# Kernel tuning notes

Measured on AMD Instinct MI355X. Metric: run time of the kernel, lower is better.

## Reference

```python
import jax, jax.numpy as jnp
import numpy as np

VOCAB = 100000
DIM = 128
B = 32768
K = 16


def setup_inputs() -> dict:
    key = jax.random.key(0)
    k1, k2, k3, k4, k5 = jax.random.split(key, 5)
    init_range = 0.5 / DIM
    word_emb = jax.random.uniform(k1, (VOCAB, DIM), jnp.float32, -init_range, init_range)
    con_emb = jax.random.uniform(k2, (VOCAB, DIM), jnp.float32, -init_range, init_range)
    centrals_words = jax.random.randint(k3, (B,), 0, VOCAB, jnp.int64 if jax.config.jax_enable_x64 else jnp.int32)
    pos_context = jax.random.randint(k4, (B,), 0, VOCAB, centrals_words.dtype)
    neg_context = jax.random.randint(k5, (B, K), 0, VOCAB, centrals_words.dtype)
    return {
        "centrals_words": centrals_words,
        "pos_context": pos_context,
        "neg_context": neg_context,
        "word_emb": word_emb,
        "con_emb": con_emb,
    }


def reference(centrals_words, pos_context, neg_context, word_emb, con_emb):
    # Gathers
    w = word_emb[centrals_words]        # [B, D]
    c = con_emb[pos_context]            # [B, D]
    n = con_emb[neg_context]            # [B, K, D]
    # Positive score: dot over D
    pos_score = jnp.sum(w * c, axis=1)              # [B]
    pos_loss = jax.nn.log_sigmoid(pos_score)        # [B]
    # Negative scores: bmm [B,K,D] @ [B,D,1] -> [B,K]
    neg_score = jnp.einsum('bkd,bd->bk', n, w)      # [B, K]
    neg_loss = jnp.sum(jax.nn.log_sigmoid(-neg_score), axis=1)  # [B]
    loss = -jnp.mean(pos_loss + neg_loss)
    return loss
```

## Files before the change

### kernel.cpp

```cpp
#include <hip/hip_runtime.h>
#include <hip/hip_fp16.h>


constexpr int Bn = 32768;
constexpr int Kn = 16;
constexpr int WPB = 4;
constexpr int NBLK = Bn / WPB;
constexpr int VOCAB = 100000;
constexpr int DIM = 128;
constexpr size_t CONV_OFF = 65536;
constexpr float SCALE = 256.0f;
constexpr float INV_SCALE = 1.0f / 256.0f;

typedef float f32x2 __attribute__((ext_vector_type(2)));

__device__ __forceinline__ float log_sigmoid_fast(float x) {
  return fminf(x, 0.0f) - __logf(1.0f + __expf(-fabsf(x)));
}

template<int M, int C>
__device__ __forceinline__ void tree_step(float* v, int lane) {
  const bool hi = (lane & M) != 0;
  const int H = C / 2;
#pragma unroll
  for (int j = 0; j < H; ++j) {
    float send = hi ? v[j] : v[j + H];
    float keep = hi ? v[j + H] : v[j];
    v[j] = keep + __shfl_xor(send, M, 64);
  }
}

__device__ __forceinline__ f32x2 dec2_fp8(unsigned short t) {
  return __builtin_amdgcn_cvt_pk_f32_fp8((int)(unsigned int)t, false);
}

__global__ __launch_bounds__(256) void convert_con(
    const float4* __restrict__ in, unsigned int* __restrict__ out, int n4)
{
  int i = blockIdx.x * 256 + threadIdx.x;
  if (i >= n4) return;
  float4 v = in[i];
  int w = 0;
  w = __builtin_amdgcn_cvt_pk_fp8_f32(v.x * SCALE, v.y * SCALE, w, false);
  w = __builtin_amdgcn_cvt_pk_fp8_f32(v.z * SCALE, v.w * SCALE, w, true);
  out[i] = (unsigned int)w;
}

__global__ __launch_bounds__(256) void skipgram_main(
    const int* __restrict__ centrals,
    const int* __restrict__ pos_ctx,
    const int* __restrict__ neg_ctx,
    const float* __restrict__ word_emb,
    const unsigned short* __restrict__ con8,
    float* __restrict__ block_sums)
{
  const int lane = threadIdx.x & 63;
  int b = blockIdx.x * WPB + (threadIdx.x >> 6);
  b = __builtin_amdgcn_readfirstlane(b);

  const float2* __restrict__ W = reinterpret_cast<const float2*>(word_emb);

  const int cw = centrals[b];
  const int pc = pos_ctx[b];
  int ni[Kn];
#pragma unroll
  for (int k = 0; k < Kn; ++k) ni[k] = neg_ctx[b * Kn + k];

  const float2 wv = W[(size_t)cw * 64 + lane];
  const unsigned short cvb = con8[(size_t)pc * 64 + lane];
  unsigned short nvb[Kn];
#pragma unroll
  for (int k = 0; k < Kn; ++k) nvb[k] = con8[(size_t)ni[k] * 64 + lane];

  float v[Kn];
#pragma unroll
  for (int k = 0; k < Kn; ++k) {
    const f32x2 nf = dec2_fp8(nvb[k]);
    v[k] = fmaf(wv.x, nf.x, wv.y * nf.y);
  }

  tree_step<1, 16>(v, lane);
  tree_step<2,  8>(v, lane);
  tree_step<4,  4>(v, lane);
  tree_step<8,  2>(v, lane);
  float s = v[0];
  s += __shfl_xor(s, 16, 64);
  s += __shfl_xor(s, 32, 64);
  s *= INV_SCALE;

  float nls = log_sigmoid_fast(-s);
  nls += __shfl_xor(nls, 1, 64);
  nls += __shfl_xor(nls, 2, 64);
  nls += __shfl_xor(nls, 4, 64);
  nls += __shfl_xor(nls, 8, 64);

  const f32x2 cf = dec2_fp8(cvb);
  float pp = fmaf(wv.x, cf.x, wv.y * cf.y);
  pp += __shfl_xor(pp,  1, 64);
  pp += __shfl_xor(pp,  2, 64);
  pp += __shfl_xor(pp,  4, 64);
  pp += __shfl_xor(pp,  8, 64);
  pp += __shfl_xor(pp, 16, 64);
  pp += __shfl_xor(pp, 32, 64);
  pp *= INV_SCALE;

  const float acc = log_sigmoid_fast(pp) + nls;

  __shared__ float smem[WPB];
  if (lane == 0) smem[threadIdx.x >> 6] = acc;
  __syncthreads();
  if (threadIdx.x == 0)
    block_sums[blockIdx.x] = (smem[0] + smem[1]) + (smem[2] + smem[3]);
}

__global__ __launch_bounds__(256) void skipgram_reduce(
    const float* __restrict__ block_sums, float* __restrict__ out)
{
  float s = 0.0f;
#pragma unroll
  for (int i = 0; i < NBLK / 256; ++i) s += block_sums[i * 256 + threadIdx.x];
  s += __shfl_xor(s,  1, 64);
  s += __shfl_xor(s,  2, 64);
  s += __shfl_xor(s,  4, 64);
  s += __shfl_xor(s,  8, 64);
  s += __shfl_xor(s, 16, 64);
  s += __shfl_xor(s, 32, 64);
  __shared__ float smem[4];
  const int lane = threadIdx.x & 63;
  if (lane == 0) smem[threadIdx.x >> 6] = s;
  __syncthreads();
  if (threadIdx.x == 0) {
    float t = (smem[0] + smem[1]) + (smem[2] + smem[3]);
    out[0] = -t * (1.0f / (float)Bn);
  }
}

extern "C" void kernel_launch(void* const* d_in, const int* in_sizes, int n_in,
                              void* d_out, int out_size, void* d_ws, size_t ws_size,
                              hipStream_t stream) {
  const int*   centrals = (const int*)d_in[0];
  const int*   pos_ctx  = (const int*)d_in[1];
  const int*   neg_ctx  = (const int*)d_in[2];
  const float* word_emb = (const float*)d_in[3];
  const float* con_emb  = (const float*)d_in[4];
  float*       out      = (float*)d_out;

  float*        block_sums = (float*)d_ws;
  unsigned int* con_fp8 = (unsigned int*)((char*)d_ws + CONV_OFF);

  const int n4 = VOCAB * DIM / 4;
  convert_con<<<(n4 + 255) / 256, 256, 0, stream>>>(
      (const float4*)con_emb, con_fp8, n4);

  skipgram_main<<<NBLK, 256, 0, stream>>>(centrals, pos_ctx, neg_ctx,
                                          word_emb,
                                          (const unsigned short*)con_fp8,
                                          block_sums);

  skipgram_reduce<<<1, 256, 0, stream>>>(block_sums, out);
}
```

Measured before the change: 138.3 us.

## Remap lanes so each 16-lane group gathers four rows with wide vector loads

The wavefront is split into four 16-lane quarters. Each quarter handles four of the sixteen negative rows, and each lane loads 8 word floats as two float4s and 8 fp8 context bytes as one uint2. Before, every lane loaded a float2 and 17 separate 2-byte fp8 values. This cuts the number of small scattered load instructions and the shuffle-tree depth. In exchange, the positive dot product is computed redundantly in every quarter and the lane-to-row selection logic gets more complex.

```diff
diff --git a/kernel.cpp b/kernel.cpp
--- a/kernel.cpp
+++ b/kernel.cpp
@@ -30,8 +30,9 @@
   }
 }
 
-__device__ __forceinline__ f32x2 dec2_fp8(unsigned short t) {
-  return __builtin_amdgcn_cvt_pk_f32_fp8((int)(unsigned int)t, false);
+template<bool HI>
+__device__ __forceinline__ f32x2 dec2(unsigned int w) {
+  return __builtin_amdgcn_cvt_pk_f32_fp8((int)w, HI);
 }
 
 __global__ __launch_bounds__(256) void convert_con(
@@ -58,7 +59,8 @@
   int b = blockIdx.x * WPB + (threadIdx.x >> 6);
   b = __builtin_amdgcn_readfirstlane(b);
 
-  const float2* __restrict__ W = reinterpret_cast<const float2*>(word_emb);
+  const int m = lane & 15;
+  const int q = lane >> 4;
 
   const int cw = centrals[b];
   const int pc = pos_ctx[b];
@@ -66,42 +68,70 @@
 #pragma unroll
   for (int k = 0; k < Kn; ++k) ni[k] = neg_ctx[b * Kn + k];
 
-  const float2 wv = W[(size_t)cw * 64 + lane];
-  const unsigned short cvb = con8[(size_t)pc * 64 + lane];
-  unsigned short nvb[Kn];
+  const bool q1 = (q & 1) != 0;
+  const bool q2 = (q & 2) != 0;
+  int rowj[4];
 #pragma unroll
-  for (int k = 0; k < Kn; ++k) nvb[k] = con8[(size_t)ni[k] * 64 + lane];
-
-  float v[Kn];
-#pragma unroll
-  for (int k = 0; k < Kn; ++k) {
-    const f32x2 nf = dec2_fp8(nvb[k]);
-    v[k] = fmaf(wv.x, nf.x, wv.y * nf.y);
+  for (int j = 0; j < 4; ++j) {
+    int t0 = q1 ? ni[4 * j + 1] : ni[4 * j + 0];
+    int t1 = q1 ? ni[4 * j + 3] : ni[4 * j + 2];
+    rowj[j] = q2 ? t1 : t0;
   }
 
-  tree_step<1, 16>(v, lane);
-  tree_step<2,  8>(v, lane);
-  tree_step<4,  4>(v, lane);
-  tree_step<8,  2>(v, lane);
+  const float4* __restrict__ Wr =
+      reinterpret_cast<const float4*>(word_emb + (size_t)cw * DIM + m * 8);
+  const float4 wa = Wr[0];
+  const float4 wb = Wr[1];
+  const uint2 pv = *reinterpret_cast<const uint2*>(con8 + (size_t)pc * 64 + m * 4);
+  uint2 nv[4];
+#pragma unroll
+  for (int j = 0; j < 4; ++j)
+    nv[j] = *reinterpret_cast<const uint2*>(con8 + (size_t)rowj[j] * 64 + m * 4);
+
+  float v[4];
+#pragma unroll
+  for (int j = 0; j < 4; ++j) {
+    const f32x2 a0 = dec2<false>(nv[j].x);
+    const f32x2 a1 = dec2<true >(nv[j].x);
+    const f32x2 a2 = dec2<false>(nv[j].y);
+    const f32x2 a3 = dec2<true >(nv[j].y);
+    v[j] = fmaf(wa.x, a0.x,
+           fmaf(wa.y, a0.y,
+           fmaf(wa.z, a1.x,
+           fmaf(wa.w, a1.y,
+           fmaf(wb.x, a2.x,
+           fmaf(wb.y, a2.y,
+           fmaf(wb.z, a3.x, wb.w * a3.y)))))));
+  }
+
+  tree_step<1, 4>(v, lane);
+  tree_step<2, 2>(v, lane);
   float s = v[0];
-  s += __shfl_xor(s, 16, 64);
-  s += __shfl_xor(s, 32, 64);
+  s += __shfl_xor(s, 4, 64);
+  s += __shfl_xor(s, 8, 64);
   s *= INV_SCALE;
 
   float nls = log_sigmoid_fast(-s);
   nls += __shfl_xor(nls, 1, 64);
   nls += __shfl_xor(nls, 2, 64);
-  nls += __shfl_xor(nls, 4, 64);
-  nls += __shfl_xor(nls, 8, 64);
+  nls += __shfl_xor(nls, 16, 64);
+  nls += __shfl_xor(nls, 32, 64);
 
-  const f32x2 cf = dec2_fp8(cvb);
-  float pp = fmaf(wv.x, cf.x, wv.y * cf.y);
-  pp += __shfl_xor(pp,  1, 64);
-  pp += __shfl_xor(pp,  2, 64);
-  pp += __shfl_xor(pp,  4, 64);
-  pp += __shfl_xor(pp,  8, 64);
-  pp += __shfl_xor(pp, 16, 64);
-  pp += __shfl_xor(pp, 32, 64);
+  const f32x2 c0 = dec2<false>(pv.x);
+  const f32x2 c1 = dec2<true >(pv.x);
+  const f32x2 c2 = dec2<false>(pv.y);
+  const f32x2 c3 = dec2<true >(pv.y);
+  float pp = fmaf(wa.x, c0.x,
+             fmaf(wa.y, c0.y,
+             fmaf(wa.z, c1.x,
+             fmaf(wa.w, c1.y,
+             fmaf(wb.x, c2.x,
+             fmaf(wb.y, c2.y,
+             fmaf(wb.z, c3.x, wb.w * c3.y)))))));
+  pp += __shfl_xor(pp, 1, 64);
+  pp += __shfl_xor(pp, 2, 64);
+  pp += __shfl_xor(pp, 4, 64);
+  pp += __shfl_xor(pp, 8, 64);
   pp *= INV_SCALE;
 
   const float acc = log_sigmoid_fast(pp) + nls;
```

Result: slower. 163.7 us (+18.4%).

## Drop fp8 con_emb conversion pass and gather fp32 rows directly with persistent waves

Applied to the files above, without the earlier changes.

Removes the per-call kernel that converted the whole 100000x128 context table to scaled fp8, and instead gathers fp32 context rows directly. Only about 18 rows per sample are touched, so the full-table read and write is avoided at the cost of larger gathered rows. The main kernel now uses a fixed grid where each wave loops over several samples, with launch bounds raised to 8 blocks per CU. It also swaps some cross-lane shuffles for DPP moves and writes per-sample partial sums that a single-block kernel reduces.

```diff
diff --git a/kernel.cpp b/kernel.cpp
--- a/kernel.cpp
+++ b/kernel.cpp
@@ -1,21 +1,28 @@
 #include <hip/hip_runtime.h>
-#include <hip/hip_fp16.h>
 
 
 constexpr int Bn = 32768;
 constexpr int Kn = 16;
 constexpr int WPB = 4;
-constexpr int NBLK = Bn / WPB;
+constexpr int NBLK = 2048;
+constexpr int NWAVE = NBLK * WPB;
+constexpr int NITER = Bn / NWAVE;
 constexpr int VOCAB = 100000;
 constexpr int DIM = 128;
-constexpr size_t CONV_OFF = 65536;
-constexpr float SCALE = 256.0f;
-constexpr float INV_SCALE = 1.0f / 256.0f;
 
 typedef float f32x2 __attribute__((ext_vector_type(2)));
 
+constexpr int XOR1 = 0xB1;
+constexpr int XOR2 = 0x4E;
+
 __device__ __forceinline__ float log_sigmoid_fast(float x) {
   return fminf(x, 0.0f) - __logf(1.0f + __expf(-fabsf(x)));
+}
+
+template<int CTRL>
+__device__ __forceinline__ float dpp_xor(float x) {
+  int r = __builtin_amdgcn_update_dpp(0, __float_as_int(x), CTRL, 0xF, 0xF, true);
+  return __int_as_float(r);
 }
 
 template<int M, int C>
@@ -30,95 +37,88 @@
   }
 }
 
-__device__ __forceinline__ f32x2 dec2_fp8(unsigned short t) {
-  return __builtin_amdgcn_cvt_pk_f32_fp8((int)(unsigned int)t, false);
+template<int M, int CTRL, int C>
+__device__ __forceinline__ void tree_step_dpp(float* v, int lane) {
+  const bool hi = (lane & M) != 0;
+  const int H = C / 2;
+#pragma unroll
+  for (int j = 0; j < H; ++j) {
+    float send = hi ? v[j] : v[j + H];
+    float keep = hi ? v[j + H] : v[j];
+    v[j] = keep + dpp_xor<CTRL>(send);
+  }
 }
 
-__global__ __launch_bounds__(256) void convert_con(
-    const float4* __restrict__ in, unsigned int* __restrict__ out, int n4)
-{
-  int i = blockIdx.x * 256 + threadIdx.x;
-  if (i >= n4) return;
-  float4 v = in[i];
-  int w = 0;
-  w = __builtin_amdgcn_cvt_pk_fp8_f32(v.x * SCALE, v.y * SCALE, w, false);
-  w = __builtin_amdgcn_cvt_pk_fp8_f32(v.z * SCALE, v.w * SCALE, w, true);
-  out[i] = (unsigned int)w;
-}
-
-__global__ __launch_bounds__(256) void skipgram_main(
+__global__ __launch_bounds__(256, 8) void skipgram_main(
     const int* __restrict__ centrals,
     const int* __restrict__ pos_ctx,
     const int* __restrict__ neg_ctx,
     const float* __restrict__ word_emb,
-    const unsigned short* __restrict__ con8,
-    float* __restrict__ block_sums)
+    const float* __restrict__ con_emb,
+    float* __restrict__ b_sums)
 {
   const int lane = threadIdx.x & 63;
-  int b = blockIdx.x * WPB + (threadIdx.x >> 6);
-  b = __builtin_amdgcn_readfirstlane(b);
+  const int wid = threadIdx.x >> 6;
+  const int gw = blockIdx.x * WPB + wid;
 
   const float2* __restrict__ W = reinterpret_cast<const float2*>(word_emb);
+  const float2* __restrict__ C = reinterpret_cast<const float2*>(con_emb);
 
-  const int cw = centrals[b];
-  const int pc = pos_ctx[b];
-  int ni[Kn];
+  for (int t = 0; t < NITER; ++t) {
+    int b = gw * NITER + t;
+    b = __builtin_amdgcn_readfirstlane(b);
+
+    const int cw = centrals[b];
+    const int pc = pos_ctx[b];
+    int ni[Kn];
 #pragma unroll
-  for (int k = 0; k < Kn; ++k) ni[k] = neg_ctx[b * Kn + k];
+    for (int k = 0; k < Kn; ++k) ni[k] = neg_ctx[b * Kn + k];
 
-  const float2 wv = W[(size_t)cw * 64 + lane];
-  const unsigned short cvb = con8[(size_t)pc * 64 + lane];
-  unsigned short nvb[Kn];
+    const float2 wv = W[(size_t)cw * 64 + lane];
+    const float2 cv = C[(size_t)pc * 64 + lane];
+    float2 nv[Kn];
 #pragma unroll
-  for (int k = 0; k < Kn; ++k) nvb[k] = con8[(size_t)ni[k] * 64 + lane];
+    for (int k = 0; k < Kn; ++k) nv[k] = C[(size_t)ni[k] * 64 + lane];
 
-  float v[Kn];
+    float v[Kn];
 #pragma unroll
-  for (int k = 0; k < Kn; ++k) {
-    const f32x2 nf = dec2_fp8(nvb[k]);
-    v[k] = fmaf(wv.x, nf.x, wv.y * nf.y);
+    for (int k = 0; k < Kn; ++k)
+      v[k] = fmaf(wv.x, nv[k].x, wv.y * nv[k].y);
+
+    tree_step_dpp<1, XOR1, 16>(v, lane);
+    tree_step_dpp<2, XOR2,  8>(v, lane);
+    tree_step<4, 4>(v, lane);
+    tree_step<8, 2>(v, lane);
+    float s = v[0];
+    s += __shfl_xor(s, 16, 64);
+    s += __shfl_xor(s, 32, 64);
+
+    float nls = log_sigmoid_fast(-s);
+    nls += dpp_xor<XOR1>(nls);
+    nls += dpp_xor<XOR2>(nls);
+    nls += __shfl_xor(nls, 4, 64);
+    nls += __shfl_xor(nls, 8, 64);
+
+    float pp = fmaf(wv.x, cv.x, wv.y * cv.y);
+    pp += dpp_xor<XOR1>(pp);
+    pp += dpp_xor<XOR2>(pp);
+    pp += __shfl_xor(pp,  4, 64);
+    pp += __shfl_xor(pp,  8, 64);
+    pp += __shfl_xor(pp, 16, 64);
+    pp += __shfl_xor(pp, 32, 64);
+
+    const float acc = log_sigmoid_fast(pp) + nls;
+
+    if (lane == 0) b_sums[b] = acc;
   }
-
-  tree_step<1, 16>(v, lane);
-  tree_step<2,  8>(v, lane);
-  tree_step<4,  4>(v, lane);
-  tree_step<8,  2>(v, lane);
-  float s = v[0];
-  s += __shfl_xor(s, 16, 64);
-  s += __shfl_xor(s, 32, 64);
-  s *= INV_SCALE;
-
-  float nls = log_sigmoid_fast(-s);
-  nls += __shfl_xor(nls, 1, 64);
-  nls += __shfl_xor(nls, 2, 64);
-  nls += __shfl_xor(nls, 4, 64);
-  nls += __shfl_xor(nls, 8, 64);
-
-  const f32x2 cf = dec2_fp8(cvb);
-  float pp = fmaf(wv.x, cf.x, wv.y * cf.y);
-  pp += __shfl_xor(pp,  1, 64);
-  pp += __shfl_xor(pp,  2, 64);
-  pp += __shfl_xor(pp,  4, 64);
-  pp += __shfl_xor(pp,  8, 64);
-  pp += __shfl_xor(pp, 16, 64);
-  pp += __shfl_xor(pp, 32, 64);
-  pp *= INV_SCALE;
-
-  const float acc = log_sigmoid_fast(pp) + nls;
-
-  __shared__ float smem[WPB];
-  if (lane == 0) smem[threadIdx.x >> 6] = acc;
-  __syncthreads();
-  if (threadIdx.x == 0)
-    block_sums[blockIdx.x] = (smem[0] + smem[1]) + (smem[2] + smem[3]);
 }
 
 __global__ __launch_bounds__(256) void skipgram_reduce(
-    const float* __restrict__ block_sums, float* __restrict__ out)
+    const float* __restrict__ b_sums, float* __restrict__ out)
 {
   float s = 0.0f;
 #pragma unroll
-  for (int i = 0; i < NBLK / 256; ++i) s += block_sums[i * 256 + threadIdx.x];
+  for (int i = 0; i < Bn / 256; ++i) s += b_sums[i * 256 + threadIdx.x];
   s += __shfl_xor(s,  1, 64);
   s += __shfl_xor(s,  2, 64);
   s += __shfl_xor(s,  4, 64);
@@ -145,17 +145,10 @@
   const float* con_emb  = (const float*)d_in[4];
   float*       out      = (float*)d_out;
 
-  float*        block_sums = (float*)d_ws;
-  unsigned int* con_fp8 = (unsigned int*)((char*)d_ws + CONV_OFF);
-
-  const int n4 = VOCAB * DIM / 4;
-  convert_con<<<(n4 + 255) / 256, 256, 0, stream>>>(
-      (const float4*)con_emb, con_fp8, n4);
+  float* b_sums = (float*)d_ws;
 
   skipgram_main<<<NBLK, 256, 0, stream>>>(centrals, pos_ctx, neg_ctx,
-                                          word_emb,
-                                          (const unsigned short*)con_fp8,
-                                          block_sums);
+                                          word_emb, con_emb, b_sums);
 
-  skipgram_reduce<<<1, 256, 0, stream>>>(block_sums, out);
+  skipgram_reduce<<<1, 256, 0, stream>>>(b_sums, out);
 }
```

Measured after the change: 148.9 us. +7.7%, slower.
